# Kernel tuning notes

Measured on AMD Instinct MI355X. Metric: run time of the kernel, lower is better.

## Reference

```python
import jax, jax.numpy as jnp
import numpy as np

B, C, D, H, W = 8, 1, 160, 160, 160
SPATIAL_AXES = (2, 3, 4)  # axial, coronal, sagittal map to dims D, H, W


def setup_inputs() -> dict:
    key = jax.random.key(0)
    k1, _ = jax.random.split(key)
    x = jax.random.normal(k1, (B, C, D, H, W), dtype=jnp.float32)
    log_sigma = jnp.zeros((3,), dtype=jnp.float32)  # log(initial_sigma=1.0)
    return {"x": x, "log_sigma": log_sigma}


def reference(x, log_sigma):
    # For each spatial axis: adjacent-slice diff, squared distance summed over
    # channel + remaining spatial dims (per batch, per slice-pair), RBF kernel,
    # then -mean over (batch, slice-pairs). Equivalent to the original
    # sum_i(-mean_b(k_i)) / (n_slices - 1) since mean is linear.
    sigma = jnp.exp(log_sigma)
    total = jnp.float32(0.0)
    for i, ax in enumerate(SPATIAL_AXES):
        d = jnp.diff(x, axis=ax)  # [B, C, ...] with S-1 along ax
        reduce_dims = tuple(a for a in range(5) if a not in (0, ax))
        sq = jnp.sum(d * d, axis=reduce_dims)  # [B, S-1]
        k = jnp.exp(-sq / (2.0 * sigma[i] ** 2))
        total = total + (-jnp.mean(k))
    return total / jnp.float32(len(SPATIAL_AXES))
```

## Files before the change

### kernel.cpp

```cpp
#include <hip/hip_runtime.h>


constexpr int Wd = 160;
constexpr int SLICE = 160 * 160;
constexpr long BSTRIDE = 160L * 25600;
constexpr int NB = 8;
constexpr int NPAIR = 159;
constexpr int WS_FLOATS = 3 * NB * NPAIR;

__global__ void zero_ws_kernel(float* __restrict__ ws) {
    int i = blockIdx.x * 256 + threadIdx.x;
    if (i < WS_FLOATS) ws[i] = 0.f;
}

__device__ __forceinline__ float sq4(const float4& a, const float4& c) {
    float e0 = a.x - c.x, e1 = a.y - c.y, e2 = a.z - c.z, e3 = a.w - c.w;
    return e0 * e0 + e1 * e1 + e2 * e2 + e3 * e3;
}

__global__ __launch_bounds__(320) void diff3_kernel(const float* __restrict__ x,
                                                    float* __restrict__ ws) {
    __shared__ float accD[10];
    __shared__ float accH[16];
    __shared__ float accW[160];

    const int t = threadIdx.x;
    const int bid = blockIdx.x;
    const int b = bid / 160;
    const int rem = bid % 160;
    const int s = rem / 10;
    const int hc = rem % 10;
    const int h0 = hc * 16;
    const int d0 = s * 10;
    const bool lastSeg = (s == 15);

    const int fw = t % 40;
    const int rp = t / 40;
    const int r1 = h0 + 2 * rp;
    const bool hOK = !(hc == 9 && rp == 7);
    const bool sOK = (fw < 39);

    if (t < 10)              accD[t] = 0.f;
    if (t >= 32 && t < 48)   accH[t - 32] = 0.f;
    if (t >= 64 && t < 224)  accW[t - 64] = 0.f;

    const float* rowA = x + (size_t)b * BSTRIDE + (size_t)d0 * SLICE
                          + (size_t)r1 * Wd + (size_t)fw * 4;

    float aW0 = 0.f, aW1 = 0.f, aW2 = 0.f, aW3 = 0.f;
    float aH1 = 0.f, aH2 = 0.f;
    float aD[10];
#pragma unroll
    for (int j = 0; j < 10; ++j) aD[j] = 0.f;

    float4 pv1, pv2;

#pragma unroll
    for (int it = 0; it < 10; ++it) {
        const float* sp = rowA + (size_t)it * SLICE;
        const float4 v1 = *(const float4*)sp;
        const float4 v2 = *(const float4*)(sp + Wd);
        float4 hv;
        if (hOK) hv = *(const float4*)(sp + 2 * Wd);
        float s1 = 0.f, s2 = 0.f;
        if (sOK) { s1 = sp[4]; s2 = sp[Wd + 4]; }

        float dw;
        dw = v1.y - v1.x; aW0 += dw * dw;
        dw = v1.z - v1.y; aW1 += dw * dw;
        dw = v1.w - v1.z; aW2 += dw * dw;
        dw = v2.y - v2.x; aW0 += dw * dw;
        dw = v2.z - v2.y; aW1 += dw * dw;
        dw = v2.w - v2.z; aW2 += dw * dw;
        if (sOK) {
            dw = s1 - v1.w; aW3 += dw * dw;
            dw = s2 - v2.w; aW3 += dw * dw;
        }
        aH1 += sq4(v2, v1);
        if (hOK) aH2 += sq4(hv, v2);
        if (it > 0) aD[it - 1] += sq4(v1, pv1) + sq4(v2, pv2);
        pv1 = v1; pv2 = v2;
    }
    if (!lastSeg) {
        const float* sp = rowA + (size_t)10 * SLICE;
        const float4 v1 = *(const float4*)sp;
        const float4 v2 = *(const float4*)(sp + Wd);
        aD[9] += sq4(v1, pv1) + sq4(v2, pv2);
    }

    __syncthreads();

    atomicAdd(&accH[r1 - h0], aH1);
    if (hOK) atomicAdd(&accH[r1 - h0 + 1], aH2);
    atomicAdd(&accW[fw * 4 + 0], aW0);
    atomicAdd(&accW[fw * 4 + 1], aW1);
    atomicAdd(&accW[fw * 4 + 2], aW2);
    if (sOK) atomicAdd(&accW[fw * 4 + 3], aW3);
#pragma unroll
    for (int j = 0; j < 10; ++j) {
        float dd = aD[j];
        for (int off = 32; off > 0; off >>= 1) dd += __shfl_down(dd, off, 64);
        if ((t & 63) == 0) atomicAdd(&accD[j], dd);
    }
    __syncthreads();

    float* wsD = ws;
    float* wsH = ws + NB * NPAIR;
    float* wsW = ws + 2 * NB * NPAIR;
    const int nd = lastSeg ? 9 : 10;
    if (t < nd) atomicAdd(&wsD[b * NPAIR + d0 + t], accD[t]);
    if (t >= 32 && t < 48) {
        int r = t - 32;
        if (h0 + r < 159) atomicAdd(&wsH[b * NPAIR + h0 + r], accH[r]);
    }
    if (t >= 64 && t < 64 + 159) {
        int k = t - 64;
        atomicAdd(&wsW[b * NPAIR + k], accW[k]);
    }
}

__global__ __launch_bounds__(256) void finalize_kernel(const float* __restrict__ ws,
                                                       const float* __restrict__ log_sigma,
                                                       float* __restrict__ out) {
    __shared__ float ssum;
    const int t = threadIdx.x;
    if (t == 0) ssum = 0.f;
    __syncthreads();

    const float f0 = -0.5f * expf(-2.f * log_sigma[0]);
    const float f1 = -0.5f * expf(-2.f * log_sigma[1]);
    const float f2 = -0.5f * expf(-2.f * log_sigma[2]);

    float acc = 0.f;
    const int n = NB * NPAIR;
    for (int i = t; i < n; i += 256) acc += expf(ws[i] * f0);
    for (int i = t; i < n; i += 256) acc += expf(ws[n + i] * f1);
    for (int i = t; i < n; i += 256) acc += expf(ws[2 * n + i] * f2);

    for (int off = 32; off > 0; off >>= 1) acc += __shfl_down(acc, off, 64);
    if ((t & 63) == 0) atomicAdd(&ssum, acc);
    __syncthreads();
    if (t == 0) out[0] = -ssum / (float)(3 * NB * NPAIR);
}

extern "C" void kernel_launch(void* const* d_in, const int* in_sizes, int n_in,
                              void* d_out, int out_size, void* d_ws, size_t ws_size,
                              hipStream_t stream) {
    const float* x = (const float*)d_in[0];
    const float* log_sigma = (const float*)d_in[1];
    float* out = (float*)d_out;
    float* ws = (float*)d_ws;

    zero_ws_kernel<<<(WS_FLOATS + 255) / 256, 256, 0, stream>>>(ws);
    diff3_kernel<<<8 * 10 * 16, 320, 0, stream>>>(x, ws);
    finalize_kernel<<<1, 256, 0, stream>>>(ws, log_sigma, out);
}
```

Measured before the change: 228.0 us.

## Tile one D-slice per block and replace global atomics with per-block partial slots

Each block now processes one full D-slice (160x160) and also reads the next slice to form the D-diff, instead of a 10-deep D segment by a 16-row H chunk. Block IDs are interleaved so that consecutive slices go to the same XCD. Per-block H and W partial sums are written to dedicated workspace slots rather than accumulated with global atomics, which removes the zeroing kernel. A new two-stage reduce sums the slots across D and applies the exponentials. The aim is to avoid global atomic contention and the zero pass. The cost is reading every slice twice (current and next, with reuse only through cache) and a heavier reduce that loops over 160 slots per key.

```diff
diff --git a/kernel.cpp b/kernel.cpp
--- a/kernel.cpp
+++ b/kernel.cpp
@@ -1,17 +1,17 @@
 #include <hip/hip_runtime.h>
 
 
-constexpr int Wd = 160;
-constexpr int SLICE = 160 * 160;
-constexpr long BSTRIDE = 160L * 25600;
+constexpr int Wd4 = 40;
+constexpr int SLICE4 = 6400;
+constexpr long BSTR4 = 160L * 6400;
 constexpr int NB = 8;
+constexpr int ND = 160;
 constexpr int NPAIR = 159;
-constexpr int WS_FLOATS = 3 * NB * NPAIR;
-
-__global__ void zero_ws_kernel(float* __restrict__ ws) {
-    int i = blockIdx.x * 256 + threadIdx.x;
-    if (i < WS_FLOATS) ws[i] = 0.f;
-}
+constexpr int NKEY = 3 * NB * NPAIR;
+constexpr int BLK_STRIDE = 384;
+constexpr int NBLK = NB * ND;
+constexpr int PART_OFF = NBLK * BLK_STRIDE;
+constexpr int NFIN = 60;
 
 __device__ __forceinline__ float sq4(const float4& a, const float4& c) {
     float e0 = a.x - c.x, e1 = a.y - c.y, e2 = a.z - c.z, e3 = a.w - c.w;
@@ -20,127 +20,110 @@
 
 __global__ __launch_bounds__(320) void diff3_kernel(const float* __restrict__ x,
                                                     float* __restrict__ ws) {
-    __shared__ float accD[10];
-    __shared__ float accH[16];
+    __shared__ float ldsH[20][321];
     __shared__ float accW[160];
+    __shared__ float accD;
 
     const int t = threadIdx.x;
     const int bid = blockIdx.x;
-    const int b = bid / 160;
-    const int rem = bid % 160;
-    const int s = rem / 10;
-    const int hc = rem % 10;
-    const int h0 = hc * 16;
-    const int d0 = s * 10;
-    const bool lastSeg = (s == 15);
+    const int xcd = bid & 7;
+    const int idx = bid >> 3;
+    const int b = idx / 20;
+    const int d = xcd * 20 + idx % 20;
+    const bool hasNext = (d < 159);
 
-    const int fw = t % 40;
-    const int rp = t / 40;
-    const int r1 = h0 + 2 * rp;
-    const bool hOK = !(hc == 9 && rp == 7);
-    const bool sOK = (fw < 39);
+    const int c4 = t % 40;
+    const int r0 = t / 40;
+    const bool sOK = (c4 < 39);
 
-    if (t < 10)              accD[t] = 0.f;
-    if (t >= 32 && t < 48)   accH[t - 32] = 0.f;
-    if (t >= 64 && t < 224)  accW[t - 64] = 0.f;
+    if (t < 160) accW[t] = 0.f;
+    if (t == 0)  accD = 0.f;
+    __syncthreads();
 
-    const float* rowA = x + (size_t)b * BSTRIDE + (size_t)d0 * SLICE
-                          + (size_t)r1 * Wd + (size_t)fw * 4;
+    const float4* curp = (const float4*)x + (size_t)b * BSTR4 + (size_t)d * SLICE4 + t;
+    const float4* nxtp = curp + SLICE4;
 
     float aW0 = 0.f, aW1 = 0.f, aW2 = 0.f, aW3 = 0.f;
-    float aH1 = 0.f, aH2 = 0.f;
-    float aD[10];
+    float aD = 0.f;
+    float aH[20];
 #pragma unroll
-    for (int j = 0; j < 10; ++j) aD[j] = 0.f;
-
-    float4 pv1, pv2;
+    for (int j = 0; j < 20; ++j) aH[j] = 0.f;
 
 #pragma unroll
-    for (int it = 0; it < 10; ++it) {
-        const float* sp = rowA + (size_t)it * SLICE;
-        const float4 v1 = *(const float4*)sp;
-        const float4 v2 = *(const float4*)(sp + Wd);
+    for (int j = 0; j < 20; ++j) {
+        const float4 v = curp[320 * j];
+        float4 nv;
+        if (hasNext) nv = nxtp[320 * j];
         float4 hv;
-        if (hOK) hv = *(const float4*)(sp + 2 * Wd);
-        float s1 = 0.f, s2 = 0.f;
-        if (sOK) { s1 = sp[4]; s2 = sp[Wd + 4]; }
+        const bool hok = (j < 19) || (r0 < 7);
+        if (hok) hv = curp[320 * j + Wd4];
+        float sb = 0.f;
+        if (sOK) sb = ((const float*)(curp + 320 * j))[4];
 
         float dw;
-        dw = v1.y - v1.x; aW0 += dw * dw;
-        dw = v1.z - v1.y; aW1 += dw * dw;
-        dw = v1.w - v1.z; aW2 += dw * dw;
-        dw = v2.y - v2.x; aW0 += dw * dw;
-        dw = v2.z - v2.y; aW1 += dw * dw;
-        dw = v2.w - v2.z; aW2 += dw * dw;
-        if (sOK) {
-            dw = s1 - v1.w; aW3 += dw * dw;
-            dw = s2 - v2.w; aW3 += dw * dw;
-        }
-        aH1 += sq4(v2, v1);
-        if (hOK) aH2 += sq4(hv, v2);
-        if (it > 0) aD[it - 1] += sq4(v1, pv1) + sq4(v2, pv2);
-        pv1 = v1; pv2 = v2;
-    }
-    if (!lastSeg) {
-        const float* sp = rowA + (size_t)10 * SLICE;
-        const float4 v1 = *(const float4*)sp;
-        const float4 v2 = *(const float4*)(sp + Wd);
-        aD[9] += sq4(v1, pv1) + sq4(v2, pv2);
+        dw = v.y - v.x; aW0 += dw * dw;
+        dw = v.z - v.y; aW1 += dw * dw;
+        dw = v.w - v.z; aW2 += dw * dw;
+        if (sOK) { dw = sb - v.w; aW3 += dw * dw; }
+        if (hok) aH[j] += sq4(hv, v);
+        if (hasNext) aD += sq4(nv, v);
     }
 
-    __syncthreads();
-
-    atomicAdd(&accH[r1 - h0], aH1);
-    if (hOK) atomicAdd(&accH[r1 - h0 + 1], aH2);
-    atomicAdd(&accW[fw * 4 + 0], aW0);
-    atomicAdd(&accW[fw * 4 + 1], aW1);
-    atomicAdd(&accW[fw * 4 + 2], aW2);
-    if (sOK) atomicAdd(&accW[fw * 4 + 3], aW3);
 #pragma unroll
-    for (int j = 0; j < 10; ++j) {
-        float dd = aD[j];
-        for (int off = 32; off > 0; off >>= 1) dd += __shfl_down(dd, off, 64);
-        if ((t & 63) == 0) atomicAdd(&accD[j], dd);
+    for (int j = 0; j < 20; ++j) ldsH[j][t] = aH[j];
+    atomicAdd(&accW[c4 * 4 + 0], aW0);
+    atomicAdd(&accW[c4 * 4 + 1], aW1);
+    atomicAdd(&accW[c4 * 4 + 2], aW2);
+    if (sOK) atomicAdd(&accW[c4 * 4 + 3], aW3);
+    if (hasNext) {
+        for (int off = 32; off > 0; off >>= 1) aD += __shfl_down(aD, off, 64);
+        if ((t & 63) == 0) atomicAdd(&accD, aD);
     }
     __syncthreads();
 
-    float* wsD = ws;
-    float* wsH = ws + NB * NPAIR;
-    float* wsW = ws + 2 * NB * NPAIR;
-    const int nd = lastSeg ? 9 : 10;
-    if (t < nd) atomicAdd(&wsD[b * NPAIR + d0 + t], accD[t]);
-    if (t >= 32 && t < 48) {
-        int r = t - 32;
-        if (h0 + r < 159) atomicAdd(&wsH[b * NPAIR + h0 + r], accH[r]);
+    float* slot = ws + (size_t)(b * ND + d) * BLK_STRIDE;
+    if (t == 0) slot[0] = accD;
+    if (t < 160) {
+        const int r = t;
+        float s = 0.f;
+        const float* src = &ldsH[r >> 3][(r & 7) * 40];
+        for (int i = 0; i < 40; ++i) s += src[i];
+        slot[1 + r] = s;
     }
-    if (t >= 64 && t < 64 + 159) {
-        int k = t - 64;
-        atomicAdd(&wsW[b * NPAIR + k], accW[k]);
-    }
+    if (t >= 160) slot[161 + (t - 160)] = accW[t - 160];
 }
 
-__global__ __launch_bounds__(256) void finalize_kernel(const float* __restrict__ ws,
-                                                       const float* __restrict__ log_sigma,
-                                                       float* __restrict__ out) {
-    __shared__ float ssum;
-    const int t = threadIdx.x;
-    if (t == 0) ssum = 0.f;
-    __syncthreads();
+__global__ __launch_bounds__(64) void reduce_kernel(const float* __restrict__ ws,
+                                                    const float* __restrict__ log_sigma,
+                                                    float* __restrict__ part) {
+    const int gk = blockIdx.x * 64 + threadIdx.x;
+    float kv = 0.f;
+    if (gk < NKEY) {
+        const int a = gk / (NB * NPAIR);
+        const int rem = gk % (NB * NPAIR);
+        const int b = rem / NPAIR;
+        const int key = rem % NPAIR;
+        const float f = -0.5f * expf(-2.f * log_sigma[a]);
+        const float* base = ws + (size_t)b * ND * BLK_STRIDE;
+        float val;
+        if (a == 0) {
+            val = base[(size_t)key * BLK_STRIDE];
+        } else {
+            const int off = (a == 1) ? (1 + key) : (161 + key);
+            val = 0.f;
+            for (int d2 = 0; d2 < ND; ++d2) val += base[d2 * BLK_STRIDE + off];
+        }
+        kv = expf(val * f);
+    }
+    for (int off = 32; off > 0; off >>= 1) kv += __shfl_down(kv, off, 64);
+    if (threadIdx.x == 0) part[blockIdx.x] = kv;
+}
 
-    const float f0 = -0.5f * expf(-2.f * log_sigma[0]);
-    const float f1 = -0.5f * expf(-2.f * log_sigma[1]);
-    const float f2 = -0.5f * expf(-2.f * log_sigma[2]);
-
-    float acc = 0.f;
-    const int n = NB * NPAIR;
-    for (int i = t; i < n; i += 256) acc += expf(ws[i] * f0);
-    for (int i = t; i < n; i += 256) acc += expf(ws[n + i] * f1);
-    for (int i = t; i < n; i += 256) acc += expf(ws[2 * n + i] * f2);
-
-    for (int off = 32; off > 0; off >>= 1) acc += __shfl_down(acc, off, 64);
-    if ((t & 63) == 0) atomicAdd(&ssum, acc);
-    __syncthreads();
-    if (t == 0) out[0] = -ssum / (float)(3 * NB * NPAIR);
+__global__ __launch_bounds__(64) void final_kernel(const float* __restrict__ part,
+                                                   float* __restrict__ out) {
+    float v = (threadIdx.x < NFIN) ? part[threadIdx.x] : 0.f;
+    for (int off = 32; off > 0; off >>= 1) v += __shfl_down(v, off, 64);
+    if (threadIdx.x == 0) out[0] = -v / (float)NKEY;
 }
 
 extern "C" void kernel_launch(void* const* d_in, const int* in_sizes, int n_in,
@@ -151,7 +134,7 @@
     float* out = (float*)d_out;
     float* ws = (float*)d_ws;
 
-    zero_ws_kernel<<<(WS_FLOATS + 255) / 256, 256, 0, stream>>>(ws);
-    diff3_kernel<<<8 * 10 * 16, 320, 0, stream>>>(x, ws);
-    finalize_kernel<<<1, 256, 0, stream>>>(ws, log_sigma, out);
+    diff3_kernel<<<NBLK, 320, 0, stream>>>(x, ws);
+    reduce_kernel<<<NFIN, 64, 0, stream>>>(ws, log_sigma, ws + PART_OFF);
+    final_kernel<<<1, 64, 0, stream>>>(ws + PART_OFF, out);
 }
```

Measured after the change: 236.6 us. 3.8% more time.
